# Kernel optimization log

Measured on AMD Instinct MI355X. Metric: run time of the kernel, lower is better.

## Reference

```python
import jax, jax.numpy as jnp
import numpy as np

S = 610      # number of HMM states (~6*nCodons+10 for nCodons=100)
E = 126      # order-transformed emission alphabet
BATCH = 32
T = 2048
NREG = 5000  # number of punished transitions
ALPHA_REG = 4.0


def setup_inputs() -> dict:
    key = jax.random.key(0)
    k1, k2, k3, k4, k5, k6 = jax.random.split(key, 6)
    obs = jax.random.randint(k1, (BATCH, T), 0, E)
    inputs = jax.nn.one_hot(obs, E, dtype=jnp.float32)          # [B,T,E]
    A = jax.nn.softmax(jax.random.normal(k2, (S, S)), axis=-1)   # row-stochastic transitions
    Bm = jax.nn.softmax(jax.random.normal(k3, (S, E)), axis=-1)  # emission matrix
    I = jax.nn.softmax(jax.random.normal(k4, (S,)))              # initial distribution
    reg_from = jax.random.randint(k5, (NREG,), 0, S)
    reg_to = jax.random.randint(k6, (NREG,), 0, S)
    return {"inputs": inputs, "A": A, "Bm": Bm, "I": I,
            "reg_from": reg_from, "reg_to": reg_to}


def reference(inputs, A, Bm, I, reg_from, reg_to):
    # emission likelihoods per step: [B,T,S]
    em = jnp.einsum('bte,se->bts', inputs, Bm)

    # HMM forward recursion with per-step normalization (scaled forward algorithm)
    alpha0 = I[None, :] * em[:, 0]                # [B,S]
    z0 = alpha0.sum(-1, keepdims=True)
    carry0 = (alpha0 / z0, jnp.log(z0[:, 0]))

    def step(carry, em_t):
        alpha, ll = carry
        a = (alpha @ A) * em_t                    # [B,S]
        z = a.sum(-1, keepdims=True)
        return (a / z, ll + jnp.log(z[:, 0])), None

    em_tbs = jnp.swapaxes(em, 0, 1)               # [T,B,S]
    (alpha_T, loglik), _ = jax.lax.scan(step, carry0, em_tbs[1:])

    loglik_mean = jnp.mean(loglik)
    # regularization: mean of log(1 - A[f, t]) over punished transitions
    reg_mean = jnp.mean(jnp.log1p(-A[reg_from, reg_to]))
    loss = -loglik_mean - ALPHA_REG * reg_mean
    return loss
```

## Files before the change

kernel.cpp:

```cpp
#include <hip/hip_runtime.h>
#include <math.h>

#define S      610
#define E      126
#define BATCH  32
#define T      2048
#define NREG   5000

#define SPAD   640
#define NT     40
#define NCH    5
#define MBXG   4
#define NBLK   8
#define THREADS 512
#define NWAVE  8
#define TPW    5
#define RT     3
#define AROW   672
#define ABUF   (MBXG * AROW)
#define ZCOL   610

typedef float f32x4 __attribute__((ext_vector_type(4)));
typedef int   i32x8 __attribute__((ext_vector_type(8)));

union Frag { uint4 q[2]; i32x8 v; };

#define MFMA_SCALED(af, bf, acc) \
    __builtin_amdgcn_mfma_scale_f32_16x16x128_f8f6f4((af), (bf), (acc), 0, 0, \
                                                     0, 0x7F7F7F7F, 0, 0x7F7F7F7F)

__device__ __forceinline__ float fastrcp(float x) {
#if __has_builtin(__builtin_amdgcn_rcpf)
    return __builtin_amdgcn_rcpf(x);
#else
    return 1.f / x;
#endif
}

__device__ __forceinline__ void ldsbar() {
#if __has_builtin(__builtin_amdgcn_s_waitcnt) && __has_builtin(__builtin_amdgcn_s_barrier)
    __builtin_amdgcn_s_waitcnt(0xC07F);
    __builtin_amdgcn_s_barrier();
#else
    __syncthreads();
#endif
}

__device__ __host__ __forceinline__ int posf(int j) {
    int n = j >> 4, mr = j & 15;
    return (n < 32) ? ((n & 7) * 16 + mr) * 4 + (n >> 3)
                    : 512 + (n - 32) * 16 + mr;
}
__device__ __forceinline__ int inv_pos(int p) {
    if (p < 512) {
        int idx = p & 3, q = p >> 2;
        return (idx * 8 + (q >> 4)) * 16 + (q & 15);
    }
    int q = p - 512;
    return (32 + (q >> 4)) * 16 + (q & 15);
}

__device__ __forceinline__ unsigned sw_e4m3_enc(float f) {
    if (!(f > 0.f)) return 0u;
    int e; float fr = frexpf(f, &e);
    if (e - 1 < -6) {
        int q = (int)rintf(f * 512.f);
        if (q > 7) q = 7;
        return (unsigned)q;
    }
    int m = (int)rintf(fr * 16.f) - 8;
    int EE = e - 1;
    if (m == 8) { m = 0; EE += 1; }
    if (EE > 8) { EE = 8; m = 7; }
    return (unsigned)(((EE + 7) << 3) | m);
}
__device__ __forceinline__ unsigned pack_quad(float v0, float v1, float v2, float v3) {
#if __has_builtin(__builtin_amdgcn_cvt_pk_fp8_f32)
    int lo = __builtin_amdgcn_cvt_pk_fp8_f32(v0, v1, 0, false);
    int hi = __builtin_amdgcn_cvt_pk_fp8_f32(v2, v3, 0, true);
    return (unsigned)(lo | hi);
#else
    return sw_e4m3_enc(v0) | (sw_e4m3_enc(v1) << 8) |
           (sw_e4m3_enc(v2) << 16) | (sw_e4m3_enc(v3) << 24);
#endif
}
__device__ __forceinline__ unsigned char fp8byte(float v) {
#if __has_builtin(__builtin_amdgcn_cvt_pk_fp8_f32)
    int w = __builtin_amdgcn_cvt_pk_fp8_f32(v, v, 0, false);
    return (unsigned char)(w & 0xFF);
#else
    return (unsigned char)sw_e4m3_enc(v);
#endif
}

__global__ void k_prep(const float* __restrict__ in, const float* __restrict__ Bm,
                       const float* __restrict__ A,
                       const int* __restrict__ rf, const int* __restrict__ rt,
                       int* __restrict__ obsT, float* __restrict__ BmT,
                       float* __restrict__ regs, unsigned* __restrict__ mx) {
    const int b = blockIdx.x, tid = threadIdx.x;
    if (b < 128) {
        for (int i = b * 256 + tid; i < E * SPAD; i += 128 * 256) {
            int o = i / SPAD, j = i - o * SPAD;
            BmT[i] = (j < S) ? Bm[j * E + o] : 0.f;
        }
    } else if (b < 384) {
        int i = (b - 128) * 256 + tid;
        if (i < BATCH * T) {
            const float2* p = (const float2*)(in + (size_t)i * E);
            int o = 0;
#pragma unroll
            for (int k = 0; k < E / 2; ++k) {
                float2 v = p[k];
                if (v.x > 0.5f) o = 2 * k;
                if (v.y > 0.5f) o = 2 * k + 1;
            }
            int bb = i / T, t = i - bb * T;
            obsT[t * BATCH + bb] = o * SPAD;
        }
    } else {
        if (tid == 0) mx[0] = 0u;
        __shared__ float wpart[4];
        float s = 0.f;
        for (int i = tid; i < NREG; i += 256)
            s += log1pf(-A[rf[i] * S + rt[i]]);
#pragma unroll
        for (int off = 1; off < 64; off <<= 1) s += __shfl_xor(s, off, 64);
        if ((tid & 63) == 0) wpart[tid >> 6] = s;
        __syncthreads();
        if (tid == 0) regs[0] = wpart[0] + wpart[1] + wpart[2] + wpart[3];
    }
}

__global__ void k_max(const float* __restrict__ A, unsigned* __restrict__ maxbuf) {
    int tid = blockIdx.x * blockDim.x + threadIdx.x;
    float m = 0.f;
    for (int i = tid; i < S * S; i += gridDim.x * blockDim.x) m = fmaxf(m, A[i]);
#pragma unroll
    for (int off = 1; off < 64; off <<= 1) m = fmaxf(m, __shfl_xor(m, off, 64));
    if ((threadIdx.x & 63) == 0) atomicMax(maxbuf, __float_as_uint(m));
}

__global__ void k_scalefin(const unsigned* __restrict__ maxbuf,
                           float* __restrict__ s_out, double* __restrict__ logs_out) {
    float mx = __uint_as_float(maxbuf[0]);
    float s = 224.f / mx;
    s_out[0] = s;
    s_out[1] = s / (float)E;
    logs_out[0] = log((double)s);
}

__global__ void k_pack8mx(const float* __restrict__ A, const float* __restrict__ s_in,
                          uint4* __restrict__ A8c) {
    int n = blockIdx.x;
    int c = blockIdx.y;
    int l = threadIdx.x;
    float s = s_in[0];
    int j = n * 16 + (l & 15);
    int pb0 = c * 128 + (l >> 4) * 32;
#pragma unroll
    for (int h = 0; h < 2; ++h) {
        unsigned dw[4];
#pragma unroll
        for (int r = 0; r < 4; ++r) {
            float v[4];
#pragma unroll
            for (int pb = 0; pb < 4; ++pb) {
                int k = inv_pos(pb0 + h * 16 + r * 4 + pb);
                v[pb] = (j == ZCOL) ? 1.0f
                      : ((k < S && j < S) ? A[k * S + j] * s : 0.f);
            }
            dw[r] = pack_quad(v[0], v[1], v[2], v[3]);
        }
        A8c[((n * NCH + c) * 2 + h) * 64 + l] = make_uint4(dw[0], dw[1], dw[2], dw[3]);
    }
}

__global__ __launch_bounds__(THREADS, 2) void k_forward(
    const uint4* __restrict__ A8c,
    const float* __restrict__ BmT,
    const int*   __restrict__ obsT,
    const float* __restrict__ Iv,
    const float* __restrict__ sbuf,
    const double* __restrict__ logs,
    double* __restrict__ ll_out)
{
    __shared__ __align__(16) uint4 pinAv[8 * NCH * 2 * 64];
    __shared__ __align__(16) unsigned char alphaq[2 * ABUF];
    __shared__ __align__(16) float zpart[NWAVE][MBXG];
    __shared__ __align__(16) float zT2[2][MBXG];
    __shared__ __align__(16) float zsc[MBXG];

    const int g    = blockIdx.x;
    const int tid  = threadIdx.x;
    const int wv   = tid >> 6;
    const int lane = tid & 63;
    const int mrow = lane & 15;
    const int quad = lane >> 4;
    const int b0   = g * MBXG;

    const float rhobar = sbuf[1];

    for (int i = tid; i < 8 * NCH * 2 * 64; i += THREADS)
        pinAv[i] = A8c[24 * NCH * 2 * 64 + i];

    i32x8 areg[RT][NCH];
#pragma unroll
    for (int rt = 0; rt < RT; ++rt)
#pragma unroll
        for (int c = 0; c < NCH; ++c) {
            Frag f;
            f.q[0] = A8c[(((rt * 8 + wv) * NCH + c) * 2 + 0) * 64 + lane];
            f.q[1] = A8c[(((rt * 8 + wv) * NCH + c) * 2 + 1) * 64 + lane];
            areg[rt][c] = f.v;
        }

    {
        const int j1 = tid + THREADS;
        const bool hasb = (j1 < SPAD);
        float Ia = (tid < S) ? Iv[tid] : 0.f;
        float Ib = (hasb && j1 < S) ? Iv[j1] : 0.f;
        float v0a[MBXG], v0b[MBXG], p0[MBXG];
#pragma unroll
        for (int m = 0; m < MBXG; ++m) {
            int o = obsT[b0 + m];
            v0a[m] = Ia * BmT[o + tid];
            v0b[m] = hasb ? Ib * BmT[o + j1] : 0.f;
            p0[m] = v0a[m] + v0b[m];
        }
#pragma unroll
        for (int off = 1; off < 64; off <<= 1)
#pragma unroll
            for (int m = 0; m < MBXG; ++m) p0[m] += __shfl_xor(p0[m], off, 64);
        if (lane == 0) {
#pragma unroll
            for (int m = 0; m < MBXG; ++m) zpart[wv][m] = p0[m];
        }
        __syncthreads();
        if (tid < MBXG) {
            float z = 0.f;
            for (int w = 0; w < NWAVE; ++w) z += zpart[w][tid];
            zsc[tid] = 128.f / z;
            zT2[0][tid] = 128.f;
        }
        __syncthreads();
        const int pa = posf(tid);
        const int pb = hasb ? posf(j1) : 0;
#pragma unroll
        for (int m = 0; m < MBXG; ++m) {
            alphaq[m * AROW + pa] = fp8byte(v0a[m] * zsc[m]);
            if (hasb) alphaq[m * AROW + pb] = fp8byte(v0b[m] * zsc[m]);
        }
        __syncthreads();
    }
    double gls = (double)__logf(zsc[quad]);

    const uint4* sp   = A8c + (size_t)((32 + wv) * NCH * 2) * 64 + lane;
    const uint4* pinp = pinAv + wv * (NCH * 2 * 64) + lane;
    const int aoff = (mrow >> 2) * AROW + quad * 32;

    int jrow[TPW];
#pragma unroll
    for (int idx = 0; idx < TPW; ++idx) {
        const int n = (idx < 4) ? (idx * 8 + wv) : (32 + wv);
        jrow[idx] = n * 16 + mrow;
    }

    int on_cur = obsT[1 * BATCH + b0 + quad];

    float em[TPW];
    i32x8 gs[3];

    for (int t = 1; t < T; ++t) {
        const int rb = (t - 1) & 1;
        const unsigned char* aqp = alphaq + rb * ABUF + aoff;
        unsigned char*       aqw = alphaq + (rb ^ 1) * ABUF;

        const int tn = (t + 1 < T) ? t + 1 : t;
        const int on_next = obsT[tn * BATCH + b0 + quad];
#pragma unroll
        for (int idx = 0; idx < TPW; ++idx) em[idx] = BmT[on_cur + jrow[idx]];
        {
            Frag f; f.q[0] = sp[0];   f.q[1] = sp[64];  gs[0] = f.v;
        }
        {
            Frag f; f.q[0] = sp[128]; f.q[1] = sp[192]; gs[1] = f.v;
        }

        i32x8 afc[2], pfc[2];
        {
            Frag f; f.q[0] = *(const uint4*)(aqp); f.q[1] = *(const uint4*)(aqp + 16);
            afc[0] = f.v;
        }
        {
            Frag f; f.q[0] = pinp[0]; f.q[1] = pinp[64]; pfc[0] = f.v;
        }

        f32x4 acc[TPW];
#pragma unroll
        for (int idx = 0; idx < TPW; ++idx) acc[idx] = (f32x4)0.f;

#pragma unroll
        for (int c = 0; c < NCH; ++c) {
            if (c + 2 < NCH) {
                Frag f;
                f.q[0] = sp[((c + 2) * 2 + 0) * 64];
                f.q[1] = sp[((c + 2) * 2 + 1) * 64];
                gs[(c + 2) % 3] = f.v;
            }
            if (c + 1 < NCH) {
                Frag f;
                f.q[0] = *(const uint4*)(aqp + (c + 1) * 128);
                f.q[1] = *(const uint4*)(aqp + (c + 1) * 128 + 16);
                afc[(c + 1) & 1] = f.v;
                Frag p;
                p.q[0] = pinp[(c + 1) * 128];
                p.q[1] = pinp[(c + 1) * 128 + 64];
                pfc[(c + 1) & 1] = p.v;
            }
            const i32x8 a = afc[c & 1];
#pragma unroll
            for (int rt = 0; rt < RT; ++rt)
                acc[rt] = MFMA_SCALED(a, areg[rt][c], acc[rt]);
            acc[3] = MFMA_SCALED(a, pfc[c & 1], acc[3]);
            acc[4] = MFMA_SCALED(a, gs[c % 3], acc[4]);
        }

        const float zps = zT2[rb][quad];
        const float zd  = fmaxf(zps * rhobar, 1e-30f);
        const float ivq = 128.f * fastrcp(zd);
        if (wv == 0) gls += (double)__logf(ivq);
#pragma unroll
        for (int idx = 0; idx < TPW; ++idx) em[idx] *= ivq;

#pragma unroll
        for (int idx = 0; idx < TPW; ++idx)
            em[idx] = acc[idx][0] * em[idx];
        {
            const int wbase = (wv * 16 + mrow) * 4;
            unsigned dw = pack_quad(em[0], em[1], em[2], em[3]);
            *(unsigned*)(aqw + quad * AROW + wbase) = dw;
            aqw[quad * AROW + 512 + wv * 16 + mrow] = fp8byte(em[4]);
        }
        if (wv == 6 && mrow == 2) zT2[rb ^ 1][quad] = acc[4][0];

        on_cur = on_next;
        ldsbar();
    }

    {
        const float zfin = zT2[(T - 1) & 1][quad];
        if (wv == 0 && mrow == 0)
            ll_out[b0 + quad] = (double)__logf(zfin) - gls - 2047.0 * logs[0];
    }
}

__global__ void k_final(const double* __restrict__ ll, const float* __restrict__ regsum,
                        float* __restrict__ out) {
    double s = 0.0;
    for (int b = 0; b < BATCH; ++b) s += ll[b];
    double loglik_mean = s / BATCH;
    double reg_mean = (double)regsum[0] / NREG;
    out[0] = (float)(-loglik_mean - 4.0 * reg_mean);
}

extern "C" void kernel_launch(void* const* d_in, const int* in_sizes, int n_in,
                              void* d_out, int out_size, void* d_ws, size_t ws_size,
                              hipStream_t stream) {
    const float* inputs = (const float*)d_in[0];
    const float* A      = (const float*)d_in[1];
    const float* Bm     = (const float*)d_in[2];
    const float* Iv     = (const float*)d_in[3];
    const int*   rf     = (const int*)d_in[4];
    const int*   rt     = (const int*)d_in[5];

    char* ws = (char*)d_ws;
    uint4*    A8c  = (uint4*)ws;
    float*    BmT  = (float*)(ws + 409600);
    int*      obsT = (int*)(ws + 732160);
    double*   ll   = (double*)(ws + 994304);
    float*    regs = (float*)(ws + 994560);
    unsigned* mx   = (unsigned*)(ws + 994564);
    float*    sbuf = (float*)(ws + 994568);
    double*   logs = (double*)(ws + 994576);

    hipLaunchKernelGGL(k_prep,     dim3(385), dim3(256), 0, stream,
                       inputs, Bm, A, rf, rt, obsT, BmT, regs, mx);
    hipLaunchKernelGGL(k_max,      dim3(256), dim3(256), 0, stream, A, mx);
    hipLaunchKernelGGL(k_scalefin, dim3(1),   dim3(1),   0, stream, mx, sbuf, logs);
    hipLaunchKernelGGL(k_pack8mx,  dim3(NT, NCH), dim3(64), 0, stream, A, sbuf, A8c);
    hipLaunchKernelGGL(k_forward,  dim3(NBLK), dim3(THREADS), 0, stream,
                       A8c, BmT, obsT, Iv, sbuf, logs, ll);
    hipLaunchKernelGGL(k_final,    dim3(1),   dim3(1),   0, stream, ll, regs, (float*)d_out);
}
```

Measured before the change: 2.265 ms.

## Ballot-based one-hot decode, zero-init MFMA first chunk, fewer prep blocks

Observation decoding now uses one wavefront per row with coalesced float2 loads and ballot/ffs to locate the hot index, replacing per-thread strided scans. This cuts uncoalesced traffic in the prep kernel and lets its grid shrink. The forward recurrence feeds a literal zero accumulator to the first MFMA chunk instead of zeroing the accumulators explicitly, which drops some register moves per step. The k_max grid is also reduced. The dominant serial forward loop is essentially unchanged, so any effect comes mostly from the small prep kernels.

```diff
diff --git a/kernel.cpp b/kernel.cpp
--- a/kernel.cpp
+++ b/kernel.cpp
@@ -104,19 +104,21 @@
             int o = i / SPAD, j = i - o * SPAD;
             BmT[i] = (j < S) ? Bm[j * E + o] : 0.f;
         }
-    } else if (b < 384) {
-        int i = (b - 128) * 256 + tid;
-        if (i < BATCH * T) {
-            const float2* p = (const float2*)(in + (size_t)i * E);
-            int o = 0;
-#pragma unroll
-            for (int k = 0; k < E / 2; ++k) {
-                float2 v = p[k];
-                if (v.x > 0.5f) o = 2 * k;
-                if (v.y > 0.5f) o = 2 * k + 1;
+    } else if (b < 192) {
+        const int lane = tid & 63;
+        const int wgl  = (b - 128) * 4 + (tid >> 6);
+        for (int row = wgl; row < BATCH * T; row += 256) {
+            float2 v = make_float2(0.f, 0.f);
+            if (lane < E / 2)
+                v = *(const float2*)(in + (size_t)row * E + lane * 2);
+            unsigned long long bx = __ballot(v.x > 0.5f);
+            unsigned long long by = __ballot(v.y > 0.5f);
+            int o = bx ? (2 * (__ffsll((long long)bx) - 1))
+                       : (2 * (__ffsll((long long)by) - 1) + 1);
+            if (lane == 0) {
+                int bb = row / T, t = row - bb * T;
+                obsT[t * BATCH + bb] = o * SPAD;
             }
-            int bb = i / T, t = i - bb * T;
-            obsT[t * BATCH + bb] = o * SPAD;
         }
     } else {
         if (tid == 0) mx[0] = 0u;
@@ -270,6 +272,7 @@
 
     float em[TPW];
     i32x8 gs[3];
+    const f32x4 zero4 = (f32x4)0.f;
 
     for (int t = 1; t < T; ++t) {
         const int rb = (t - 1) & 1;
@@ -297,8 +300,6 @@
         }
 
         f32x4 acc[TPW];
-#pragma unroll
-        for (int idx = 0; idx < TPW; ++idx) acc[idx] = (f32x4)0.f;
 
 #pragma unroll
         for (int c = 0; c < NCH; ++c) {
@@ -319,11 +320,19 @@
                 pfc[(c + 1) & 1] = p.v;
             }
             const i32x8 a = afc[c & 1];
-#pragma unroll
-            for (int rt = 0; rt < RT; ++rt)
-                acc[rt] = MFMA_SCALED(a, areg[rt][c], acc[rt]);
-            acc[3] = MFMA_SCALED(a, pfc[c & 1], acc[3]);
-            acc[4] = MFMA_SCALED(a, gs[c % 3], acc[4]);
+            if (c == 0) {
+#pragma unroll
+                for (int rt = 0; rt < RT; ++rt)
+                    acc[rt] = MFMA_SCALED(a, areg[rt][0], zero4);
+                acc[3] = MFMA_SCALED(a, pfc[0], zero4);
+                acc[4] = MFMA_SCALED(a, gs[0], zero4);
+            } else {
+#pragma unroll
+                for (int rt = 0; rt < RT; ++rt)
+                    acc[rt] = MFMA_SCALED(a, areg[rt][c], acc[rt]);
+                acc[3] = MFMA_SCALED(a, pfc[c & 1], acc[3]);
+                acc[4] = MFMA_SCALED(a, gs[c % 3], acc[4]);
+            }
         }
 
         const float zps = zT2[rb][quad];
@@ -384,9 +393,9 @@
     float*    sbuf = (float*)(ws + 994568);
     double*   logs = (double*)(ws + 994576);
 
-    hipLaunchKernelGGL(k_prep,     dim3(385), dim3(256), 0, stream,
+    hipLaunchKernelGGL(k_prep,     dim3(193), dim3(256), 0, stream,
                        inputs, Bm, A, rf, rt, obsT, BmT, regs, mx);
-    hipLaunchKernelGGL(k_max,      dim3(256), dim3(256), 0, stream, A, mx);
+    hipLaunchKernelGGL(k_max,      dim3(64),  dim3(256), 0, stream, A, mx);
     hipLaunchKernelGGL(k_scalefin, dim3(1),   dim3(1),   0, stream, mx, sbuf, logs);
     hipLaunchKernelGGL(k_pack8mx,  dim3(NT, NCH), dim3(64), 0, stream, A, sbuf, A8c);
     hipLaunchKernelGGL(k_forward,  dim3(NBLK), dim3(THREADS), 0, stream,
```

Measured after the change: 2.268 ms. No clear change (+0.1%).
